# Kernel optimization log

Measured on AMD Instinct MI355X. Metric: run time of the kernel, lower is better.

The kernel has to match this reference:

```python
import jax, jax.numpy as jnp
import numpy as np
from jax import lax


def setup_inputs() -> dict:
    key = jax.random.key(0)
    I = jax.random.uniform(key, (32, 3, 512, 512), dtype=jnp.float32)
    return {"I": I, "k": 15}


def reference(I, k):
    # Channel-wise min -> dark channel (torch does this via -max_pool over transposed channel dim)
    dark = jnp.min(I, axis=1, keepdims=True)  # [B,1,H,W]
    p = k // 2
    # Spatial min-pool kxk, stride 1, pad k//2. torch max_pool2d pads with -inf,
    # so the min-pool equivalent pads with +inf: reduce_window with min and +inf init.
    eroded = lax.reduce_window(
        dark,
        jnp.inf,
        lax.min,
        window_dimensions=(1, 1, k, k),
        window_strides=(1, 1, 1, 1),
        padding=[(0, 0), (0, 0), (p, p), (p, p)],
    )
    return eroded
```

## Files before the change

kernel.cpp:

```cpp
#include <hip/hip_runtime.h>
#include <math.h>

#define BATCH 32
#define CH    3
#define H     512
#define W     512
#define KWIN  15
#define PAD   7
#define TROWS 8

__global__ __launch_bounds__(256) void dark_hmin(const float* __restrict__ I,
                                                 float* __restrict__ tmp) {
    const int bh = blockIdx.x;
    const int b  = bh >> 9;
    const int h  = bh & (H - 1);
    const int t  = threadIdx.x;

    __shared__ float s[W + 2 * PAD];

    const float* row0 = I + ((size_t)(b * CH + 0) * H + h) * W;
    const float* row1 = I + ((size_t)(b * CH + 1) * H + h) * W;
    const float* row2 = I + ((size_t)(b * CH + 2) * H + h) * W;

    const int x = t * 2;
    float2 a0 = *(const float2*)(row0 + x);
    float2 a1 = *(const float2*)(row1 + x);
    float2 a2 = *(const float2*)(row2 + x);
    s[PAD + x]     = fminf(fminf(a0.x, a1.x), a2.x);
    s[PAD + x + 1] = fminf(fminf(a0.y, a1.y), a2.y);
    if (t < PAD) {
        s[t]           = INFINITY;
        s[PAD + W + t] = INFINITY;
    }
    __syncthreads();

    float common = s[x + 1];
    #pragma unroll
    for (int j = 2; j < KWIN; ++j) common = fminf(common, s[x + j]);
    float m0 = fminf(common, s[x]);
    float m1 = fminf(common, s[x + KWIN]);

    float2 o; o.x = m0; o.y = m1;
    *(float2*)(tmp + ((size_t)b * H + h) * W + x) = o;
}

__global__ __launch_bounds__(256) void vmin(const float* __restrict__ tmp,
                                            float* __restrict__ out) {
    const int x  = blockIdx.x * 256 + threadIdx.x;
    const int y0 = blockIdx.y * TROWS;
    const int b  = blockIdx.z;

    const float* col = tmp + (size_t)b * H * W + x;

    float v[TROWS + KWIN - 1];
    #pragma unroll
    for (int i = 0; i < TROWS + KWIN - 1; ++i) {
        const int y = y0 - PAD + i;
        v[i] = (y >= 0 && y < H) ? col[(size_t)y * W] : INFINITY;
    }

    float* o = out + (size_t)b * H * W + x;
    #pragma unroll
    for (int r = 0; r < TROWS; ++r) {
        float m = v[r];
        #pragma unroll
        for (int j = 1; j < KWIN; ++j) m = fminf(m, v[r + j]);
        o[(size_t)(y0 + r) * W] = m;
    }
}

extern "C" void kernel_launch(void* const* d_in, const int* in_sizes, int n_in,
                              void* d_out, int out_size, void* d_ws, size_t ws_size,
                              hipStream_t stream) {
    const float* I   = (const float*)d_in[0];
    float* out = (float*)d_out;
    float* tmp = (float*)d_ws;

    dark_hmin<<<dim3(BATCH * H), dim3(256), 0, stream>>>(I, tmp);
    vmin<<<dim3(W / 256, H / TROWS, BATCH), dim3(256), 0, stream>>>(tmp, out);
}
```

Before: 169.6 us.

## Fuse dark-channel and separable min-pool into one kernel with a shared-memory ring buffer

Replaces the two-kernel pipeline with a single kernel. The old pipeline ran a channel-min plus horizontal min pass into a workspace, then a separate vertical min pass. Now each block handles 32 output rows of one image, computes horizontal mins row by row into a 15-row shared-memory ring, and takes the vertical min from that ring. This removes the intermediate global write and read plus one launch. In exchange it re-reads 14 halo input rows per block, runs a serial per-row loop with several block barriers, and launches only 512 blocks, so it risks being bound by latency and low occupancy.

```diff
diff --git a/kernel.cpp b/kernel.cpp
--- a/kernel.cpp
+++ b/kernel.cpp
@@ -7,75 +7,88 @@
 #define W     512
 #define KWIN  15
 #define PAD   7
-#define TROWS 8
+#define TH    32
 
-__global__ __launch_bounds__(256) void dark_hmin(const float* __restrict__ I,
-                                                 float* __restrict__ tmp) {
-    const int bh = blockIdx.x;
-    const int b  = bh >> 9;
-    const int h  = bh & (H - 1);
+__global__ __launch_bounds__(256) void dcp_fused(const float* __restrict__ I,
+                                                 float* __restrict__ out) {
+    const int b  = blockIdx.y;
+    const int y0 = blockIdx.x * TH;
     const int t  = threadIdx.x;
+    const int x  = t * 2;
 
-    __shared__ float s[W + 2 * PAD];
+    __shared__ float ring[KWIN][W];
+    __shared__ float s[W + 2 * PAD + 2];
 
-    const float* row0 = I + ((size_t)(b * CH + 0) * H + h) * W;
-    const float* row1 = I + ((size_t)(b * CH + 1) * H + h) * W;
-    const float* row2 = I + ((size_t)(b * CH + 2) * H + h) * W;
+    const float* base = I + (size_t)b * CH * H * W;
 
-    const int x = t * 2;
-    float2 a0 = *(const float2*)(row0 + x);
-    float2 a1 = *(const float2*)(row1 + x);
-    float2 a2 = *(const float2*)(row2 + x);
-    s[PAD + x]     = fminf(fminf(a0.x, a1.x), a2.x);
-    s[PAD + x + 1] = fminf(fminf(a0.y, a1.y), a2.y);
-    if (t < PAD) {
-        s[t]           = INFINITY;
-        s[PAD + W + t] = INFINITY;
-    }
-    __syncthreads();
+    auto insert_row = [&](int y) {
+        const int slot = (y + PAD) % KWIN;
+        if (y >= 0 && y < H) {
+            const float2 a0 = *(const float2*)(base + ((size_t)(0 * H) + y) * W + x);
+            const float2 a1 = *(const float2*)(base + ((size_t)(1 * H) + y) * W + x);
+            const float2 a2 = *(const float2*)(base + ((size_t)(2 * H) + y) * W + x);
+            s[PAD + x]     = fminf(fminf(a0.x, a1.x), a2.x);
+            s[PAD + x + 1] = fminf(fminf(a0.y, a1.y), a2.y);
+            if (t < PAD) {
+                s[t]           = INFINITY;
+                s[PAD + W + t] = INFINITY;
+            }
+            __syncthreads();
+            const float p0 = fminf(s[x + 1],  s[x + 2]);
+            const float p1 = fminf(s[x + 3],  s[x + 4]);
+            const float p2 = fminf(s[x + 5],  s[x + 6]);
+            const float p3 = fminf(s[x + 7],  s[x + 8]);
+            const float p4 = fminf(s[x + 9],  s[x + 10]);
+            const float p5 = fminf(s[x + 11], s[x + 12]);
+            const float p6 = fminf(s[x + 13], s[x + 14]);
+            const float q0 = fminf(p0, p1), q1 = fminf(p2, p3), q2 = fminf(p4, p5);
+            const float common = fminf(fminf(q0, q1), fminf(q2, p6));
+            ring[slot][x]     = fminf(common, s[x]);
+            ring[slot][x + 1] = fminf(common, s[x + KWIN]);
+        } else {
+            ring[slot][x]     = INFINITY;
+            ring[slot][x + 1] = INFINITY;
+        }
+    };
 
-    float common = s[x + 1];
-    #pragma unroll
-    for (int j = 2; j < KWIN; ++j) common = fminf(common, s[x + j]);
-    float m0 = fminf(common, s[x]);
-    float m1 = fminf(common, s[x + KWIN]);
-
-    float2 o; o.x = m0; o.y = m1;
-    *(float2*)(tmp + ((size_t)b * H + h) * W + x) = o;
-}
-
-__global__ __launch_bounds__(256) void vmin(const float* __restrict__ tmp,
-                                            float* __restrict__ out) {
-    const int x  = blockIdx.x * 256 + threadIdx.x;
-    const int y0 = blockIdx.y * TROWS;
-    const int b  = blockIdx.z;
-
-    const float* col = tmp + (size_t)b * H * W + x;
-
-    float v[TROWS + KWIN - 1];
-    #pragma unroll
-    for (int i = 0; i < TROWS + KWIN - 1; ++i) {
-        const int y = y0 - PAD + i;
-        v[i] = (y >= 0 && y < H) ? col[(size_t)y * W] : INFINITY;
+    #pragma unroll 1
+    for (int i = 0; i < KWIN - 1; ++i) {
+        insert_row(y0 - PAD + i);
+        __syncthreads();
     }
 
-    float* o = out + (size_t)b * H * W + x;
-    #pragma unroll
-    for (int r = 0; r < TROWS; ++r) {
-        float m = v[r];
+    #pragma unroll 1
+    for (int r = 0; r < TH; ++r) {
+        const int y = y0 + r;
+        insert_row(y + PAD);
+        __syncthreads();
+
+        float2 v[KWIN];
         #pragma unroll
-        for (int j = 1; j < KWIN; ++j) m = fminf(m, v[r + j]);
-        o[(size_t)(y0 + r) * W] = m;
+        for (int i = 0; i < KWIN; ++i) v[i] = *(const float2*)&ring[i][x];
+        float mx0 = fminf(v[0].x, v[1].x),  my0 = fminf(v[0].y, v[1].y);
+        float mx1 = fminf(v[2].x, v[3].x),  my1 = fminf(v[2].y, v[3].y);
+        float mx2 = fminf(v[4].x, v[5].x),  my2 = fminf(v[4].y, v[5].y);
+        float mx3 = fminf(v[6].x, v[7].x),  my3 = fminf(v[6].y, v[7].y);
+        float mx4 = fminf(v[8].x, v[9].x),  my4 = fminf(v[8].y, v[9].y);
+        float mx5 = fminf(v[10].x, v[11].x), my5 = fminf(v[10].y, v[11].y);
+        float mx6 = fminf(v[12].x, v[13].x), my6 = fminf(v[12].y, v[13].y);
+        mx0 = fminf(mx0, mx1); my0 = fminf(my0, my1);
+        mx2 = fminf(mx2, mx3); my2 = fminf(my2, my3);
+        mx4 = fminf(mx4, mx5); my4 = fminf(my4, my5);
+        mx6 = fminf(mx6, v[14].x); my6 = fminf(my6, v[14].y);
+        float2 o;
+        o.x = fminf(fminf(mx0, mx2), fminf(mx4, mx6));
+        o.y = fminf(fminf(my0, my2), fminf(my4, my6));
+        *(float2*)(out + ((size_t)b * H + y) * W + x) = o;
+        __syncthreads();
     }
 }
 
 extern "C" void kernel_launch(void* const* d_in, const int* in_sizes, int n_in,
                               void* d_out, int out_size, void* d_ws, size_t ws_size,
                               hipStream_t stream) {
-    const float* I   = (const float*)d_in[0];
+    const float* I = (const float*)d_in[0];
     float* out = (float*)d_out;
-    float* tmp = (float*)d_ws;
-
-    dark_hmin<<<dim3(BATCH * H), dim3(256), 0, stream>>>(I, tmp);
-    vmin<<<dim3(W / 256, H / TROWS, BATCH), dim3(256), 0, stream>>>(tmp, out);
+    dcp_fused<<<dim3(H / TH, BATCH), dim3(256), 0, stream>>>(I, out);
 }
```

Result: slower. 177.3 us (+4.5%).

## Fuse channel-min, vertical and horizontal min passes into one tiled kernel

Applied to the files above, without the earlier changes.

Replaces the two-kernel pipeline (channel-min plus horizontal min into a workspace, then a vertical min pass) with a single kernel. Each block handles 8 output rows of one image. It computes the vertical 15-row min in registers using a shared prefix/suffix scheme over the 22 needed rows, stores the 8 results in shared memory, and then does the horizontal min from shared memory. This removes the write and re-read of the intermediate tensor and one launch. In exchange, each block re-reads 14 halo rows of the 3-channel input, about 2.75x read amplification on the input.

```diff
diff --git a/kernel.cpp b/kernel.cpp
--- a/kernel.cpp
+++ b/kernel.cpp
@@ -7,75 +7,85 @@
 #define W     512
 #define KWIN  15
 #define PAD   7
-#define TROWS 8
+#define TH    8
 
-__global__ __launch_bounds__(256) void dark_hmin(const float* __restrict__ I,
-                                                 float* __restrict__ tmp) {
-    const int bh = blockIdx.x;
-    const int b  = bh >> 9;
-    const int h  = bh & (H - 1);
+__global__ __launch_bounds__(256, 8) void dcp_fused2(const float* __restrict__ I,
+                                                     float* __restrict__ out) {
+    const int b  = blockIdx.y;
+    const int y0 = blockIdx.x * TH;
     const int t  = threadIdx.x;
+    const int x  = t * 2;
 
-    __shared__ float s[W + 2 * PAD];
+    __shared__ float tile[TH][W + 2 * PAD + 2];
 
-    const float* row0 = I + ((size_t)(b * CH + 0) * H + h) * W;
-    const float* row1 = I + ((size_t)(b * CH + 1) * H + h) * W;
-    const float* row2 = I + ((size_t)(b * CH + 2) * H + h) * W;
+    const float* base = I + (size_t)b * CH * H * W;
 
-    const int x = t * 2;
-    float2 a0 = *(const float2*)(row0 + x);
-    float2 a1 = *(const float2*)(row1 + x);
-    float2 a2 = *(const float2*)(row2 + x);
-    s[PAD + x]     = fminf(fminf(a0.x, a1.x), a2.x);
-    s[PAD + x + 1] = fminf(fminf(a0.y, a1.y), a2.y);
+    auto load_cm = [&](int y) -> float2 {
+        float2 r;
+        if (y < 0 || y >= H) { r.x = INFINITY; r.y = INFINITY; return r; }
+        const float2 a0 = *(const float2*)(base + ((size_t)0 * H + y) * W + x);
+        const float2 a1 = *(const float2*)(base + ((size_t)1 * H + y) * W + x);
+        const float2 a2 = *(const float2*)(base + ((size_t)2 * H + y) * W + x);
+        r.x = fminf(fminf(a0.x, a1.x), a2.x);
+        r.y = fminf(fminf(a0.y, a1.y), a2.y);
+        return r;
+    };
+
+    float2 P[PAD];
+    {
+        float2 run = load_cm(y0 + 8);
+        P[0] = run;
+        #pragma unroll
+        for (int k = 1; k < PAD; ++k) {
+            const float2 c = load_cm(y0 + 8 + k);
+            run.x = fminf(run.x, c.x); run.y = fminf(run.y, c.y);
+            P[k] = run;
+        }
+    }
+    float2 U = load_cm(y0 + 7);
+    #pragma unroll
+    for (int i = 13; i >= 8; --i) {
+        const float2 c = load_cm(y0 - PAD + i);
+        U.x = fminf(U.x, c.x); U.y = fminf(U.y, c.y);
+    }
+    #pragma unroll
+    for (int i = PAD; i >= 0; --i) {
+        const float2 c = load_cm(y0 - PAD + i);
+        U.x = fminf(U.x, c.x); U.y = fminf(U.y, c.y);
+        float2 o;
+        if (i > 0) { o.x = fminf(U.x, P[i - 1].x); o.y = fminf(U.y, P[i - 1].y); }
+        else       { o = U; }
+        *(float2*)&tile[i][PAD + x] = o;
+    }
+
     if (t < PAD) {
-        s[t]           = INFINITY;
-        s[PAD + W + t] = INFINITY;
+        #pragma unroll
+        for (int r = 0; r < TH; ++r) tile[r][t] = INFINITY;
+    } else if (t < 2 * PAD) {
+        #pragma unroll
+        for (int r = 0; r < TH; ++r) tile[r][W + t] = INFINITY;
     }
     __syncthreads();
 
-    float common = s[x + 1];
     #pragma unroll
-    for (int j = 2; j < KWIN; ++j) common = fminf(common, s[x + j]);
-    float m0 = fminf(common, s[x]);
-    float m1 = fminf(common, s[x + KWIN]);
-
-    float2 o; o.x = m0; o.y = m1;
-    *(float2*)(tmp + ((size_t)b * H + h) * W + x) = o;
-}
-
-__global__ __launch_bounds__(256) void vmin(const float* __restrict__ tmp,
-                                            float* __restrict__ out) {
-    const int x  = blockIdx.x * 256 + threadIdx.x;
-    const int y0 = blockIdx.y * TROWS;
-    const int b  = blockIdx.z;
-
-    const float* col = tmp + (size_t)b * H * W + x;
-
-    float v[TROWS + KWIN - 1];
-    #pragma unroll
-    for (int i = 0; i < TROWS + KWIN - 1; ++i) {
-        const int y = y0 - PAD + i;
-        v[i] = (y >= 0 && y < H) ? col[(size_t)y * W] : INFINITY;
-    }
-
-    float* o = out + (size_t)b * H * W + x;
-    #pragma unroll
-    for (int r = 0; r < TROWS; ++r) {
-        float m = v[r];
+    for (int r = 0; r < TH; ++r) {
+        float2 w[8];
         #pragma unroll
-        for (int j = 1; j < KWIN; ++j) m = fminf(m, v[r + j]);
-        o[(size_t)(y0 + r) * W] = m;
+        for (int j = 0; j < 8; ++j) w[j] = *(const float2*)&tile[r][x + 2 * j];
+        float m = fminf(w[0].y, w[7].x);
+        #pragma unroll
+        for (int j = 1; j < 7; ++j) m = fminf(m, fminf(w[j].x, w[j].y));
+        float2 o;
+        o.x = fminf(m, w[0].x);
+        o.y = fminf(m, w[7].y);
+        *(float2*)(out + ((size_t)b * H + y0 + r) * W + x) = o;
     }
 }
 
 extern "C" void kernel_launch(void* const* d_in, const int* in_sizes, int n_in,
                               void* d_out, int out_size, void* d_ws, size_t ws_size,
                               hipStream_t stream) {
-    const float* I   = (const float*)d_in[0];
+    const float* I = (const float*)d_in[0];
     float* out = (float*)d_out;
-    float* tmp = (float*)d_ws;
-
-    dark_hmin<<<dim3(BATCH * H), dim3(256), 0, stream>>>(I, tmp);
-    vmin<<<dim3(W / 256, H / TROWS, BATCH), dim3(256), 0, stream>>>(tmp, out);
+    dcp_fused2<<<dim3(H / TH, BATCH), dim3(256), 0, stream>>>(I, out);
 }
```

Result: slower. 176.4 us (+4.0%).

## Fuse dark channel, horizontal and vertical min into one wave-level kernel

Applied to the files above, without the earlier changes.

Replaces the two-kernel pipeline (channel-min plus horizontal min into a workspace, then vertical min) with one kernel. Each 64-lane wave handles a 112-column strip of 16 output rows. The horizontal 15-wide min is built from cross-lane shuffles, and the vertical min uses a prefix/suffix (van Herk style) scheme over 30 rows. This removes the intermediate global write and read and one launch, at the cost of redundant halo loads (30 input rows per 16 output rows, plus overlapping strip columns).

```diff
diff --git a/kernel.cpp b/kernel.cpp
--- a/kernel.cpp
+++ b/kernel.cpp
@@ -1,81 +1,83 @@
 #include <hip/hip_runtime.h>
 #include <math.h>
 
-#define BATCH 32
-#define CH    3
-#define H     512
-#define W     512
-#define KWIN  15
-#define PAD   7
-#define TROWS 8
+#define BATCH  32
+#define CH     3
+#define H      512
+#define W      512
+#define KWIN   15
+#define PAD    7
+#define TH     16
+#define NRR    (TH + KWIN - 1)
+#define STRIP  112
+#define NSTRIP 5
+#define NWAVES (BATCH * (H / TH) * NSTRIP)
 
-__global__ __launch_bounds__(256) void dark_hmin(const float* __restrict__ I,
-                                                 float* __restrict__ tmp) {
-    const int bh = blockIdx.x;
-    const int b  = bh >> 9;
-    const int h  = bh & (H - 1);
-    const int t  = threadIdx.x;
-
-    __shared__ float s[W + 2 * PAD];
-
-    const float* row0 = I + ((size_t)(b * CH + 0) * H + h) * W;
-    const float* row1 = I + ((size_t)(b * CH + 1) * H + h) * W;
-    const float* row2 = I + ((size_t)(b * CH + 2) * H + h) * W;
-
-    const int x = t * 2;
-    float2 a0 = *(const float2*)(row0 + x);
-    float2 a1 = *(const float2*)(row1 + x);
-    float2 a2 = *(const float2*)(row2 + x);
-    s[PAD + x]     = fminf(fminf(a0.x, a1.x), a2.x);
-    s[PAD + x + 1] = fminf(fminf(a0.y, a1.y), a2.y);
-    if (t < PAD) {
-        s[t]           = INFINITY;
-        s[PAD + W + t] = INFINITY;
-    }
-    __syncthreads();
-
-    float common = s[x + 1];
-    #pragma unroll
-    for (int j = 2; j < KWIN; ++j) common = fminf(common, s[x + j]);
-    float m0 = fminf(common, s[x]);
-    float m1 = fminf(common, s[x + KWIN]);
-
-    float2 o; o.x = m0; o.y = m1;
-    *(float2*)(tmp + ((size_t)b * H + h) * W + x) = o;
+static __device__ __forceinline__ float2 min2(float2 a, float2 b) {
+    float2 r;
+    r.x = fminf(a.x, b.x);
+    r.y = fminf(a.y, b.y);
+    return r;
 }
 
-__global__ __launch_bounds__(256) void vmin(const float* __restrict__ tmp,
-                                            float* __restrict__ out) {
-    const int x  = blockIdx.x * 256 + threadIdx.x;
-    const int y0 = blockIdx.y * TROWS;
-    const int b  = blockIdx.z;
+__global__ void dcp_fused6(const float* __restrict__ I, float* __restrict__ out) {
+    const int wid = blockIdx.x * 4 + (threadIdx.x >> 6);
+    const int L   = threadIdx.x & 63;
+    const int s   = wid % NSTRIP;
+    const int rb  = (wid / NSTRIP) % (H / TH);
+    const int b   = wid / (NSTRIP * (H / TH));
+    const int y0  = rb * TH;
+    const int f   = s * STRIP - 8 + 2 * L;
+    const int cl  = min(max(f, 0), W - 2);
+    const bool cv = (f >= 0) && (f < W);
+    const bool st = (L >= 4) && (L <= 59) && (f < W);
 
-    const float* col = tmp + (size_t)b * H * W + x;
+    const float* base = I + (size_t)b * CH * H * W + cl;
+    float* outb = out + (size_t)b * H * W;
 
-    float v[TROWS + KWIN - 1];
+    auto hrow = [&](int i) -> float2 {
+        const int y = y0 - PAD + i;
+        float2 wv;
+        if (y >= 0 && y < H) {
+            const float* p = base + (size_t)y * W;
+            const float2 A = *(const float2*)(p);
+            const float2 Bv = *(const float2*)(p + (size_t)H * W);
+            const float2 Cv = *(const float2*)(p + (size_t)2 * H * W);
+            float2 d = min2(min2(A, Bv), Cv);
+            if (!cv) { d.x = INFINITY; d.y = INFINITY; }
+            const float pm = fminf(d.x, d.y);
+            const float t2 = fminf(pm, __shfl_down(pm, 1));
+            const float t4 = fminf(t2, __shfl_down(t2, 2));
+            const float q7 = fminf(t4, __shfl_up(t4, 3));
+            wv.x = fminf(q7, __shfl_up(d.y, 4));
+            wv.y = fminf(q7, __shfl_down(d.x, 4));
+        } else {
+            wv.x = INFINITY; wv.y = INFINITY;
+        }
+        return wv;
+    };
+
+    float2 P[KWIN];
+    P[0] = hrow(KWIN);
     #pragma unroll
-    for (int i = 0; i < TROWS + KWIN - 1; ++i) {
-        const int y = y0 - PAD + i;
-        v[i] = (y >= 0 && y < H) ? col[(size_t)y * W] : INFINITY;
+    for (int j = 1; j < KWIN; ++j) P[j] = min2(P[j - 1], hrow(KWIN + j));
+    if (st) *(float2*)(outb + (size_t)(y0 + 15) * W + f) = P[KWIN - 1];
+
+    float2 U = hrow(14);
+    if (st) *(float2*)(outb + (size_t)(y0 + 14) * W + f) = min2(U, P[13]);
+    #pragma unroll
+    for (int r = 13; r >= 1; --r) {
+        U = min2(U, hrow(r));
+        if (st) *(float2*)(outb + (size_t)(y0 + r) * W + f) = min2(U, P[r - 1]);
     }
-
-    float* o = out + (size_t)b * H * W + x;
-    #pragma unroll
-    for (int r = 0; r < TROWS; ++r) {
-        float m = v[r];
-        #pragma unroll
-        for (int j = 1; j < KWIN; ++j) m = fminf(m, v[r + j]);
-        o[(size_t)(y0 + r) * W] = m;
-    }
+    U = min2(U, hrow(0));
+    if (st) *(float2*)(outb + (size_t)y0 * W + f) = U;
 }
 
 extern "C" void kernel_launch(void* const* d_in, const int* in_sizes, int n_in,
                               void* d_out, int out_size, void* d_ws, size_t ws_size,
                               hipStream_t stream) {
-    const float* I   = (const float*)d_in[0];
+    const float* I = (const float*)d_in[0];
     float* out = (float*)d_out;
-    float* tmp = (float*)d_ws;
-
-    dark_hmin<<<dim3(BATCH * H), dim3(256), 0, stream>>>(I, tmp);
-    vmin<<<dim3(W / 256, H / TROWS, BATCH), dim3(256), 0, stream>>>(tmp, out);
+    dcp_fused6<<<dim3(NWAVES / 4), dim3(256), 0, stream>>>(I, out);
 }
```

After: 166.6 us. No clear change (-1.8%).
